# Kernel optimization log

Hardware: AMD Instinct MI355X
Metric: run time of the kernel (lower is better)

## Reference

```python
import jax, jax.numpy as jnp
import numpy as np

LAMBDA_SOFTMAX = 9.0
LAMBDA_LSE = 6.0
EPS = 1e-8
LEAKY_SLOPE = 0.1


def setup_inputs() -> dict:
    key = jax.random.key(0)
    k1, k2, k3, k4 = jax.random.split(key, 4)
    B, R, L, D = 256, 36, 40, 1024  # n_image=n_caption=B, n_regions, max_words, embed
    return {
        'pool_img': jax.random.normal(k1, (B, D), jnp.float32),
        'img_emb': jax.random.normal(k2, (B, R, D), jnp.float32),
        'pool_txt': jax.random.normal(k3, (B, D), jnp.float32),
        'cap_emb': jax.random.normal(k4, (B, L, D), jnp.float32),
    }


def _l2norm(x, axis):
    return x / (jnp.sqrt(jnp.sum(x * x, axis=axis, keepdims=True)) + EPS)


def _lse_reduce(m):
    # mul_(lambda_lse).exp_() ; sum over singleton dim ; log / lambda_lse
    return jnp.log(jnp.exp(m * LAMBDA_LSE)) / LAMBDA_LSE


def _text_score_one(cap_i, txt_poo_i, images):
    # cap_i: (L, d) query; images: (B, R, d) context. clipped_l2norm variant.
    attn = jnp.einsum('brd,ld->brl', images, cap_i)            # (B, R, L)
    attn = jax.nn.leaky_relu(attn, LEAKY_SLOPE)
    attn = _l2norm(attn, axis=2)                               # l2norm over queryL
    attn = jnp.swapaxes(attn, 1, 2)                            # (B, L, R)
    attn = jax.nn.softmax(attn * LAMBDA_SOFTMAX, axis=-1)      # softmax over regions
    wctx = jnp.einsum('blr,brd->bld', attn, images)            # (B, L, d)
    w12 = jnp.einsum('bld,d->bl', wctx, txt_poo_i)
    w1 = jnp.sqrt(jnp.sum(txt_poo_i * txt_poo_i))
    w2 = jnp.sqrt(jnp.sum(wctx * wctx, axis=2))
    sim = w12 / jnp.maximum(w1 * w2, EPS)                      # (B, L)
    return _lse_reduce(jnp.mean(sim, axis=1))                  # (B,)


def _image_score_one(cap_i, img_emb, img_poo):
    # query: img_emb (B, R, d); context: cap_i (L, d) broadcast over B.
    attn = jnp.einsum('ld,brd->blr', cap_i, img_emb)           # (B, L, R)
    attn = jax.nn.leaky_relu(attn, LEAKY_SLOPE)
    attn = _l2norm(attn, axis=2)                               # l2norm over regions
    attn = jnp.swapaxes(attn, 1, 2)                            # (B, R, L)
    attn = jax.nn.softmax(attn * LAMBDA_SOFTMAX, axis=-1)      # softmax over words
    wctx = jnp.einsum('brl,ld->brd', attn, cap_i)              # (B, R, d)
    w12 = jnp.einsum('brd,bd->br', wctx, img_poo)
    w1 = jnp.sqrt(jnp.sum(img_poo * img_poo, axis=1, keepdims=True))  # (B,1)
    w2 = jnp.sqrt(jnp.sum(wctx * wctx, axis=2))                # (B, R)
    sim = w12 / jnp.maximum(w1 * w2, EPS)
    return _lse_reduce(jnp.mean(sim, axis=1))                  # (B,)


def reference(pool_img, img_emb, pool_txt, cap_emb):
    # scores_t2i: loop over captions -> vmap; result (n_cap, n_image) -> transpose
    t2i = jax.vmap(_text_score_one, in_axes=(0, 0, None))(cap_emb, pool_txt, img_emb).T
    i2t = jax.vmap(_image_score_one, in_axes=(0, None, None))(cap_emb, img_emb, pool_img).T
    base = pool_img @ pool_txt.T
    return t2i + i2t + base
```

## Files before the change

### kernel.cpp

```cpp
#include <hip/hip_runtime.h>

typedef unsigned short u16;
typedef __attribute__((ext_vector_type(8))) short bf16x8;
typedef __attribute__((ext_vector_type(4))) float f32x4;
typedef __attribute__((ext_vector_type(4))) unsigned u32x4;

#define D_EMB 1024
#define NBAT  256
#define AS1 __attribute__((address_space(1)))
#define AS3 __attribute__((address_space(3)))

__device__ __forceinline__ u16 f2bf(float f){
    unsigned int u = __float_as_uint(f);
    unsigned int r = (u + 0x7fffu + ((u >> 16) & 1u)) >> 16;
    return (u16)r;
}
__device__ __forceinline__ float leaky(float x){ return x > 0.f ? x : 0.1f * x; }

__device__ __forceinline__ unsigned pack2(float a, float b){
    return (__float_as_uint(a) >> 16) | (__float_as_uint(b) & 0xffff0000u);
}

__global__ void pack_kernel(const float* __restrict__ pool_img, const float* __restrict__ img_emb,
                            const float* __restrict__ pool_txt, const float* __restrict__ cap_emb,
                            u16* __restrict__ imgw, u16* __restrict__ capw){
    int row = blockIdx.x;
    const float* src; u16* dst;
    if (row < NBAT * 37){
        int e = row / 37, rr = row - e * 37;
        src = (rr < 36) ? (img_emb + ((size_t)e * 36 + rr) * D_EMB) : (pool_img + (size_t)e * D_EMB);
        dst = imgw + (size_t)row * D_EMB;
    } else {
        int r2 = row - NBAT * 37;
        int e = r2 / 41, rr = r2 - e * 41;
        src = (rr < 40) ? (cap_emb + ((size_t)e * 40 + rr) * D_EMB) : (pool_txt + (size_t)e * D_EMB);
        dst = capw + (size_t)r2 * D_EMB;
    }
    int t = threadIdx.x;
    float4 v = ((const float4*)src)[t];
    unsigned long long pk = (unsigned long long)f2bf(v.x)
        | ((unsigned long long)f2bf(v.y) << 16)
        | ((unsigned long long)f2bf(v.z) << 32)
        | ((unsigned long long)f2bf(v.w) << 48);
    *(unsigned long long*)(dst + (size_t)t * 4) = pk;
}

__global__ void norm_kernel(const float* __restrict__ pool_img, const float* __restrict__ pool_txt,
                            float* __restrict__ w1i, float* __restrict__ w1t){
    __shared__ float red[256];
    int v = blockIdx.x;
    const float* src = (v < 256) ? (pool_img + (size_t)v * D_EMB)
                                 : (pool_txt + (size_t)(v - 256) * D_EMB);
    int t = threadIdx.x;
    float4 x = ((const float4*)src)[t];
    red[t] = x.x*x.x + x.y*x.y + x.z*x.z + x.w*x.w;
    __syncthreads();
    for (int off = 128; off > 0; off >>= 1){
        if (t < off) red[t] += red[t + off];
        __syncthreads();
    }
    if (t == 0){
        float n = sqrtf(red[0]);
        if (v < 256) w1i[v] = n; else w1t[v - 256] = n;
    }
}

__launch_bounds__(256, 2)
__global__ void gram_kernel(const u16* __restrict__ imgw, const u16* __restrict__ capw,
                            float* __restrict__ G, float* __restrict__ H){
    __shared__ __align__(16) char gsm[6144];
    int blk = blockIdx.x;
    int tid = threadIdx.x, lane = tid & 63;
    int wave = __builtin_amdgcn_readfirstlane(tid >> 6);
    int frow = lane & 15, q = lane >> 4;

    const u16* E; float* Gout; int R;
    if (blk < NBAT){ E = imgw + (size_t)blk * 37 * D_EMB; Gout = G + (size_t)blk * 1296; R = 36; }
    else { int b = blk - NBAT; E = capw + (size_t)b * 41 * D_EMB; Gout = H + (size_t)b * 1600; R = 40; }

    {
        uint4 z = {0u,0u,0u,0u};
        for (int off = tid * 16; off < 6144; off += 4096) *(uint4*)(gsm + off) = z;
    }

    const u16* gsrc[2]; int goff[2]; bool gval[2];
    #pragma unroll
    for (int j = 0; j < 2; ++j){
        int g = wave + j * 4;
        gval[j] = false; gsrc[j] = E; goff[j] = 0;
        if (g < 6){
            int kk = g / 3, t = g - kk * 3;
            int row = t * 16 + frow;
            gsrc[j] = E + (size_t)row * D_EMB + kk * 32 + q * 8;
            goff[j] = g * 1024;
            gval[j] = (row < R);
        }
    }

    int wm = wave >> 1, wn = wave & 1;
    int nTm = wm ? 1 : 2, nTn = wn ? 1 : 2;
    f32x4 acc[2][2];
    #pragma unroll
    for (int a = 0; a < 2; ++a)
        #pragma unroll
        for (int b = 0; b < 2; ++b) acc[a][b] = (f32x4){0.f,0.f,0.f,0.f};

    for (int c = 0; c < 16; ++c){
        __syncthreads();
        #pragma unroll
        for (int j = 0; j < 2; ++j){
            if (gval[j]){
                __builtin_amdgcn_global_load_lds(
                    (const AS1 void*)(const void*)(gsrc[j] + c * 64),
                    (AS3 void*)(void*)(gsm + goff[j] + lane * 16),
                    16, 0, 0);
            }
        }
        __syncthreads();
        #pragma unroll
        for (int kk = 0; kk < 2; ++kk){
            bf16x8 fA[2], fB[2];
            #pragma unroll
            for (int mi = 0; mi < 2; ++mi)
                if (mi < nTm) fA[mi] = *(const bf16x8*)(gsm + ((kk * 3 + (wm + mi * 2)) * 64 + lane) * 16);
            #pragma unroll
            for (int ni = 0; ni < 2; ++ni)
                if (ni < nTn) fB[ni] = *(const bf16x8*)(gsm + ((kk * 3 + (wn + ni * 2)) * 64 + lane) * 16);
            #pragma unroll
            for (int mi = 0; mi < 2; ++mi)
                if (mi < nTm)
                    #pragma unroll
                    for (int ni = 0; ni < 2; ++ni)
                        if (ni < nTn)
                            acc[mi][ni] = __builtin_amdgcn_mfma_f32_16x16x32_bf16(
                                fA[mi], fB[ni], acc[mi][ni], 0, 0, 0);
        }
    }

    #pragma unroll
    for (int mi = 0; mi < 2; ++mi){
        if (mi < nTm){
            int tm = wm + mi * 2;
            #pragma unroll
            for (int ni = 0; ni < 2; ++ni){
                if (ni < nTn){
                    int tn = wn + ni * 2;
                    int col = tn * 16 + frow;
                    if (col < R){
                        #pragma unroll
                        for (int g = 0; g < 4; ++g){
                            int row = tm * 16 + q * 4 + g;
                            if (row < R) Gout[row * R + col] = acc[mi][ni][g];
                        }
                    }
                }
            }
        }
    }
}

template<int R>
__device__ __forceinline__ void chol_wave(const float* __restrict__ src,
                                          u16* __restrict__ dst, int lane){
    int r = lane;
    bool act = (r < R);
    const float* row = src + (size_t)(act ? r : 0) * R;
    float a[R];
    #pragma unroll
    for (int k = 0; k < R; ++k) a[k] = act ? row[k] : 0.f;
    #pragma unroll
    for (int j = 0; j < R; ++j){
        float ajj = __shfl(a[j], j);
        float inv = (ajj > 1e-12f) ? rsqrtf(ajj) : 0.f;
        float lrj = a[j] * inv;
        if (r < j || !act) lrj = 0.f;
        dst[j * 64 + lane] = f2bf(lrj);
        #pragma unroll
        for (int k = j + 1; k < R; ++k){
            float lkj = __shfl(lrj, k);
            a[k] = fmaf(-lrj, lkj, a[k]);
        }
    }
    #pragma unroll
    for (int j = R; j < 48; ++j) dst[j * 64 + lane] = 0;
}

__global__ void chol_kernel(const float* __restrict__ G, const float* __restrict__ H,
                            u16* __restrict__ Lbi, u16* __restrict__ Lbc){
    int lane = threadIdx.x & 63;
    int wave = threadIdx.x >> 6;
    int id = blockIdx.x * 4 + wave;
    if (id < NBAT) chol_wave<36>(G + (size_t)id * 1296, Lbi + (size_t)id * 3072, lane);
    else           chol_wave<40>(H + (size_t)(id - NBAT) * 1600, Lbc + (size_t)(id - NBAT) * 3072, lane);
}

__launch_bounds__(256, 5)
__global__ void fused_kernel(const u16* __restrict__ imgw, const u16* __restrict__ capw,
                             const u16* __restrict__ Lbi, const u16* __restrict__ Lbc,
                             const float* __restrict__ w1i, const float* __restrict__ w1t,
                             float* __restrict__ out){
    __shared__ __align__(16) char smem[26624];
    float* Call = (float*)smem;
    float* rnb  = (float*)(smem + 25160);
    float* cnb  = (float*)(smem + 25736);

    int tid  = threadIdx.x;
    int lane = tid & 63;
    int wave = __builtin_amdgcn_readfirstlane(tid >> 6);
    int frow = lane & 15, q = lane >> 4;

    int lin = blockIdx.x;
    int xcd = lin & 7;
    int s   = lin >> 3;
    int b_t = (xcd << 4) | (s & 15);
    int i_t = s >> 4;
    int b0 = b_t * 2, i0 = i_t * 2;
    const u16* Ag = imgw + (size_t)b0 * 37 * D_EMB;
    const u16* Bg = capw + (size_t)i0 * 41 * D_EMB;

    {
        uint4 z = {0u,0u,0u,0u};
        for (int off = tid * 16; off < 22528; off += 4096) *(uint4*)(smem + off) = z;
    }

    const u16* gsrc[3]; int goff[3]; bool gval[3];
    #pragma unroll
    for (int j = 0; j < 3; ++j){
        int g = wave + j * 4;
        gval[j] = false; gsrc[j] = Ag; goff[j] = 0;
        if (g < 11){
            if (g < 5){
                int row = g * 16 + frow;
                gsrc[j] = Ag + (size_t)row * D_EMB + q * 8;
                goff[j] = g * 1024;
                gval[j] = (row < 74);
            } else {
                int gb = g - 5;
                int row = gb * 16 + frow;
                gsrc[j] = Bg + (size_t)row * D_EMB + q * 8;
                goff[j] = 5120 + gb * 1024;
                gval[j] = (row < 82);
            }
        }
    }

    int wm = wave >> 1, wn = wave & 1;
    int nTm = wm ? 2 : 3;
    f32x4 acc[3][3];
    #pragma unroll
    for (int aa = 0; aa < 3; ++aa)
        #pragma unroll
        for (int bb = 0; bb < 3; ++bb) acc[aa][bb] = (f32x4){0.f, 0.f, 0.f, 0.f};

    __syncthreads();

    #pragma unroll
    for (int j = 0; j < 3; ++j){
        if (gval[j]){
            __builtin_amdgcn_global_load_lds(
                (const AS1 void*)(const void*)(gsrc[j]),
                (AS3 void*)(void*)(smem + goff[j] + lane * 16),
                16, 0, 0);
        }
    }
    __syncthreads();

    for (int c = 0; c < 32; ++c){
        if (c < 31){
            int nb = ((c + 1) & 1) * 11264;
            #pragma unroll
            for (int j = 0; j < 3; ++j){
                if (gval[j]){
                    __builtin_amdgcn_global_load_lds(
                        (const AS1 void*)(const void*)(gsrc[j] + (c + 1) * 32),
                        (AS3 void*)(void*)(smem + nb + goff[j] + lane * 16),
                        16, 0, 0);
                }
            }
        }
        int cb = (c & 1) * 11264;
        bf16x8 bfr[3];
        #pragma unroll
        for (int ni = 0; ni < 3; ++ni){
            int tn = wn + ni * 2;
            bfr[ni] = *(const bf16x8*)(smem + cb + 5120 + tn * 1024 + lane * 16);
        }
        #pragma unroll
        for (int mi = 0; mi < 3; ++mi){
            if (mi < nTm){
                int tm = wm + mi * 2;
                bf16x8 af = *(const bf16x8*)(smem + cb + tm * 1024 + lane * 16);
                #pragma unroll
                for (int ni = 0; ni < 3; ++ni){
                    acc[mi][ni] = __builtin_amdgcn_mfma_f32_16x16x32_bf16(
                        af, bfr[ni], acc[mi][ni], 0, 0, 0);
                }
            }
        }
        __syncthreads();
    }

    #pragma unroll
    for (int mi = 0; mi < 3; ++mi){
        if (mi < nTm){
            int tm = wm + mi * 2;
            #pragma unroll
            for (int ni = 0; ni < 3; ++ni){
                int tn = wn + ni * 2;
                int col = tn * 16 + frow;
                int rbase = tm * 16 + q * 4;
                if (col < 82){
                    #pragma unroll
                    for (int g = 0; g < 4; ++g){
                        int rowc = rbase + g;
                        if (rowc < 74) Call[rowc * 85 + col] = acc[mi][ni][g];
                    }
                }
            }
        }
    }
    __syncthreads();

    int pb = wave >> 1, pi = wave & 1;
    int bg = b0 + pb, ig = i0 + pi;
    const float* Sv = Call + (pb * 37) * 85 + pi * 41;
    const u16* Lb_t2i = Lbi + (size_t)bg * 3072;
    const u16* Lb_i2t = Lbc + (size_t)ig * 3072;

    {
        int r0 = (lane < 36) ? lane : 35;
        float s2 = 0.f;
        #pragma unroll
        for (int l = 0; l < 40; ++l){ float x = leaky(Sv[r0 * 85 + l]); s2 = fmaf(x, x, s2); }
        if (lane < 36) rnb[wave * 36 + lane] = 1.f / (sqrtf(s2) + 1e-8f);
    }
    {
        int l0 = (lane < 40) ? lane : 39;
        float s2 = 0.f;
        #pragma unroll
        for (int r = 0; r < 36; ++r){ float x = leaky(Sv[r * 85 + l0]); s2 = fmaf(x, x, s2); }
        if (lane < 40) cnb[wave * 40 + lane] = 1.f / (sqrtf(s2) + 1e-8f);
    }
    float base = Sv[36 * 85 + 40];

    float tsum;
    {
        f32x4 pacc[3][3];
        #pragma unroll
        for (int aa = 0; aa < 3; ++aa)
            #pragma unroll
            for (int bb = 0; bb < 3; ++bb) pacc[aa][bb] = (f32x4){0.f,0.f,0.f,0.f};
        #pragma unroll
        for (int kk = 0; kk < 2; ++kk){
            float rn[8];
            #pragma unroll
            for (int j = 0; j < 8; ++j){
                int k = kk * 32 + q * 8 + j;
                int kc = (k < 36) ? k : 35;
                rn[j] = (k < 36) ? rnb[wave * 36 + kc] : 0.f;
            }
            u32x4 pw;
            #pragma unroll
            for (int jj = 0; jj < 4; ++jj){
                int k0 = kk * 32 + q * 8 + jj * 2, k1 = k0 + 1;
                int c0 = (k0 < 36) ? k0 : 35, c1 = (k1 < 36) ? k1 : 35;
                float p0 = (k0 < 36) ? Sv[c0 * 85 + 40] : 0.f;
                float p1 = (k1 < 36) ? Sv[c1 * 85 + 40] : 0.f;
                pw[jj] = pack2(p0, p1);
            }
            bf16x8 afr[3];
            #pragma unroll
            for (int mt = 0; mt < 3; ++mt){
                int m = mt * 16 + frow;
                u32x4 aw;
                #pragma unroll
                for (int jj = 0; jj < 4; ++jj){
                    int k0 = kk * 32 + q * 8 + jj * 2, k1 = k0 + 1;
                    int c0 = (k0 < 36) ? k0 : 35, c1 = (k1 < 36) ? k1 : 35;
                    float e0 = __expf(9.f * leaky(Sv[c0 * 85 + m]) * rn[jj * 2]);
                    float e1 = __expf(9.f * leaky(Sv[c1 * 85 + m]) * rn[jj * 2 + 1]);
                    e0 = (k0 < 36) ? e0 : 0.f;
                    e1 = (k1 < 36) ? e1 : 0.f;
                    aw[jj] = pack2(e0, e1);
                }
                afr[mt] = __builtin_bit_cast(bf16x8, aw);
            }
            #pragma unroll
            for (int nt = 0; nt < 3; ++nt){
                bf16x8 bfr = *(const bf16x8*)(Lb_t2i + (nt * 16 + frow) * 64 + kk * 32 + q * 8);
                if (nt == 2 && frow == 4) bfr = __builtin_bit_cast(bf16x8, pw);
                #pragma unroll
                for (int mt = 0; mt < 3; ++mt)
                    pacc[mt][nt] = __builtin_amdgcn_mfma_f32_16x16x32_bf16(
                        afr[mt], bfr, pacc[mt][nt], 0, 0, 0);
            }
        }
        float w1 = w1t[ig];
        tsum = 0.f;
        #pragma unroll
        for (int mt = 0; mt < 3; ++mt){
            #pragma unroll
            for (int g = 0; g < 4; ++g){
                float sv = pacc[mt][0][g] * pacc[mt][0][g]
                         + pacc[mt][1][g] * pacc[mt][1][g];
                float t2 = pacc[mt][2][g] * pacc[mt][2][g];
                sv += (frow < 4) ? t2 : 0.f;
                sv += __shfl_xor(sv, 1); sv += __shfl_xor(sv, 2);
                sv += __shfl_xor(sv, 4); sv += __shfl_xor(sv, 8);
                float nm = __shfl(pacc[mt][2][g], (lane & 48) + 4);
                int m = mt * 16 + 4 * q + g;
                float sim = nm / fmaxf(w1 * sqrtf(sv), 1e-8f);
                tsum += (m < 40) ? sim : 0.f;
            }
        }
        tsum += __shfl_xor(tsum, 16);
        tsum += __shfl_xor(tsum, 32);
    }

    float isum;
    {
        f32x4 pacc[3][3];
        #pragma unroll
        for (int aa = 0; aa < 3; ++aa)
            #pragma unroll
            for (int bb = 0; bb < 3; ++bb) pacc[aa][bb] = (f32x4){0.f,0.f,0.f,0.f};
        #pragma unroll
        for (int kk = 0; kk < 2; ++kk){
            float cn[8];
            #pragma unroll
            for (int j = 0; j < 8; ++j){
                int k = kk * 32 + q * 8 + j;
                int kc = (k < 40) ? k : 39;
                cn[j] = (k < 40) ? cnb[wave * 40 + kc] : 0.f;
            }
            u32x4 qw;
            #pragma unroll
            for (int jj = 0; jj < 4; ++jj){
                int k0 = kk * 32 + q * 8 + jj * 2, k1 = k0 + 1;
                int c0 = (k0 < 40) ? k0 : 39, c1 = (k1 < 40) ? k1 : 39;
                float q0 = (k0 < 40) ? Sv[36 * 85 + c0] : 0.f;
                float q1 = (k1 < 40) ? Sv[36 * 85 + c1] : 0.f;
                qw[jj] = pack2(q0, q1);
            }
            bf16x8 afr[3];
            #pragma unroll
            for (int mt = 0; mt < 3; ++mt){
                int m = mt * 16 + frow;
                int mr = (m < 36) ? m : 35;
                u32x4 aw;
                #pragma unroll
                for (int jj = 0; jj < 4; ++jj){
                    int k0 = kk * 32 + q * 8 + jj * 2, k1 = k0 + 1;
                    int c0 = (k0 < 40) ? k0 : 39, c1 = (k1 < 40) ? k1 : 39;
                    float e0 = __expf(9.f * leaky(Sv[mr * 85 + c0]) * cn[jj * 2]);
                    float e1 = __expf(9.f * leaky(Sv[mr * 85 + c1]) * cn[jj * 2 + 1]);
                    e0 = (k0 < 40) ? e0 : 0.f;
                    e1 = (k1 < 40) ? e1 : 0.f;
                    aw[jj] = pack2(e0, e1);
                }
                afr[mt] = __builtin_bit_cast(bf16x8, aw);
            }
            #pragma unroll
            for (int nt = 0; nt < 3; ++nt){
                bf16x8 bfr = *(const bf16x8*)(Lb_i2t + (nt * 16 + frow) * 64 + kk * 32 + q * 8);
                if (nt == 2 && frow == 8) bfr = __builtin_bit_cast(bf16x8, qw);
                #pragma unroll
                for (int mt = 0; mt < 3; ++mt)
                    pacc[mt][nt] = __builtin_amdgcn_mfma_f32_16x16x32_bf16(
                        afr[mt], bfr, pacc[mt][nt], 0, 0, 0);
            }
        }
        float w1 = w1i[bg];
        isum = 0.f;
        #pragma unroll
        for (int mt = 0; mt < 3; ++mt){
            #pragma unroll
            for (int g = 0; g < 4; ++g){
                float sv = pacc[mt][0][g] * pacc[mt][0][g]
                         + pacc[mt][1][g] * pacc[mt][1][g];
                float t2 = pacc[mt][2][g] * pacc[mt][2][g];
                sv += (frow < 8) ? t2 : 0.f;
                sv += __shfl_xor(sv, 1); sv += __shfl_xor(sv, 2);
                sv += __shfl_xor(sv, 4); sv += __shfl_xor(sv, 8);
                float nm = __shfl(pacc[mt][2][g], (lane & 48) + 8);
                int m = mt * 16 + 4 * q + g;
                float sim = nm / fmaxf(w1 * sqrtf(sv), 1e-8f);
                isum += (m < 36) ? sim : 0.f;
            }
        }
        isum += __shfl_xor(isum, 16);
        isum += __shfl_xor(isum, 32);
    }

    if (lane == 0)
        out[bg * 256 + ig] = tsum * (1.f / 40.f) + isum * (1.f / 36.f) + base;
}

extern "C" void kernel_launch(void* const* d_in, const int* in_sizes, int n_in,
                              void* d_out, int out_size, void* d_ws, size_t ws_size,
                              hipStream_t stream){
    const float* pool_img = (const float*)d_in[0];
    const float* img_emb  = (const float*)d_in[1];
    const float* pool_txt = (const float*)d_in[2];
    const float* cap_emb  = (const float*)d_in[3];
    float* out = (float*)d_out;

    char* ws = (char*)d_ws;
    size_t o = 0;
    u16* imgw = (u16*)(ws + o);  o += (size_t)256 * 37 * 1024 * 2;
    u16* capw = (u16*)(ws + o);  o += (size_t)256 * 41 * 1024 * 2;
    float* G  = (float*)(ws + o); o += (size_t)256 * 36 * 36 * 4;
    float* H  = (float*)(ws + o); o += (size_t)256 * 40 * 40 * 4;
    float* w1i = (float*)(ws + o); o += 1024;
    float* w1t = (float*)(ws + o); o += 1024;
    u16* Lbi = (u16*)(ws + o); o += (size_t)256 * 48 * 64 * 2;
    u16* Lbc = (u16*)(ws + o); o += (size_t)256 * 48 * 64 * 2;

    pack_kernel<<<19968, 256, 0, stream>>>(pool_img, img_emb, pool_txt, cap_emb, imgw, capw);
    norm_kernel<<<512, 256, 0, stream>>>(pool_img, pool_txt, w1i, w1t);
    gram_kernel<<<512, 256, 0, stream>>>(imgw, capw, G, H);
    chol_kernel<<<128, 256, 0, stream>>>(G, H, Lbi, Lbc);
    fused_kernel<<<16384, 256, 0, stream>>>(imgw, capw, Lbi, Lbc, w1i, w1t, out);
}
```

Measured before the change: 809.5 us.

## Fuse pool norms into pack, widen fused GEMM K-step, fold softmax scale

Computes the pooled-vector norms inside pack_kernel, which removes the separate norm kernel launch. Rewrites the fused kernel's main loop to load 64-wide K chunks, two MFMA k-slices per stage, in 16 iterations with single buffering instead of 32 double-buffered steps, so there are fewer barriers but less load/compute overlap. It also folds the softmax factor of 9 into the reciprocal norms, removing a multiply per exp. A clamp on the column index guards the out-of-range row reads.

```diff
diff --git a/kernel.cpp b/kernel.cpp
--- a/kernel.cpp
+++ b/kernel.cpp
@@ -23,18 +23,25 @@
 
 __global__ void pack_kernel(const float* __restrict__ pool_img, const float* __restrict__ img_emb,
                             const float* __restrict__ pool_txt, const float* __restrict__ cap_emb,
-                            u16* __restrict__ imgw, u16* __restrict__ capw){
+                            u16* __restrict__ imgw, u16* __restrict__ capw,
+                            float* __restrict__ w1i, float* __restrict__ w1t){
+    __shared__ float red[256];
     int row = blockIdx.x;
     const float* src; u16* dst;
+    bool is_pool; float* wout;
     if (row < NBAT * 37){
         int e = row / 37, rr = row - e * 37;
+        is_pool = (rr == 36);
         src = (rr < 36) ? (img_emb + ((size_t)e * 36 + rr) * D_EMB) : (pool_img + (size_t)e * D_EMB);
         dst = imgw + (size_t)row * D_EMB;
+        wout = w1i + e;
     } else {
         int r2 = row - NBAT * 37;
         int e = r2 / 41, rr = r2 - e * 41;
+        is_pool = (rr == 40);
         src = (rr < 40) ? (cap_emb + ((size_t)e * 40 + rr) * D_EMB) : (pool_txt + (size_t)e * D_EMB);
         dst = capw + (size_t)r2 * D_EMB;
+        wout = w1t + e;
     }
     int t = threadIdx.x;
     float4 v = ((const float4*)src)[t];
@@ -43,25 +50,14 @@
         | ((unsigned long long)f2bf(v.z) << 32)
         | ((unsigned long long)f2bf(v.w) << 48);
     *(unsigned long long*)(dst + (size_t)t * 4) = pk;
-}
-
-__global__ void norm_kernel(const float* __restrict__ pool_img, const float* __restrict__ pool_txt,
-                            float* __restrict__ w1i, float* __restrict__ w1t){
-    __shared__ float red[256];
-    int v = blockIdx.x;
-    const float* src = (v < 256) ? (pool_img + (size_t)v * D_EMB)
-                                 : (pool_txt + (size_t)(v - 256) * D_EMB);
-    int t = threadIdx.x;
-    float4 x = ((const float4*)src)[t];
-    red[t] = x.x*x.x + x.y*x.y + x.z*x.z + x.w*x.w;
-    __syncthreads();
-    for (int off = 128; off > 0; off >>= 1){
-        if (t < off) red[t] += red[t + off];
+    if (is_pool){
+        red[t] = v.x*v.x + v.y*v.y + v.z*v.z + v.w*v.w;
         __syncthreads();
-    }
-    if (t == 0){
-        float n = sqrtf(red[0]);
-        if (v < 256) w1i[v] = n; else w1t[v - 256] = n;
+        for (int off = 128; off > 0; off >>= 1){
+            if (t < off) red[t] += red[t + off];
+            __syncthreads();
+        }
+        if (t == 0) *wout = sqrtf(red[0]);
     }
 }
 
@@ -223,22 +219,24 @@
         for (int off = tid * 16; off < 22528; off += 4096) *(uint4*)(smem + off) = z;
     }
 
-    const u16* gsrc[3]; int goff[3]; bool gval[3];
-    #pragma unroll
-    for (int j = 0; j < 3; ++j){
+    const u16* gsrc[6]; int goff[6]; bool gval[6];
+    #pragma unroll
+    for (int j = 0; j < 6; ++j){
         int g = wave + j * 4;
         gval[j] = false; gsrc[j] = Ag; goff[j] = 0;
-        if (g < 11){
-            if (g < 5){
-                int row = g * 16 + frow;
-                gsrc[j] = Ag + (size_t)row * D_EMB + q * 8;
+        if (g < 22){
+            if (g < 10){
+                int tm = g % 5, kk = g / 5;
+                int row = tm * 16 + frow;
+                gsrc[j] = Ag + (size_t)row * D_EMB + kk * 32 + q * 8;
                 goff[j] = g * 1024;
                 gval[j] = (row < 74);
             } else {
-                int gb = g - 5;
-                int row = gb * 16 + frow;
-                gsrc[j] = Bg + (size_t)row * D_EMB + q * 8;
-                goff[j] = 5120 + gb * 1024;
+                int gb = g - 10;
+                int tn = gb % 6, kk = gb / 6;
+                int row = tn * 16 + frow;
+                gsrc[j] = Bg + (size_t)row * D_EMB + kk * 32 + q * 8;
+                goff[j] = 10240 + gb * 1024;
                 gval[j] = (row < 82);
             }
         }
@@ -252,53 +250,41 @@
         #pragma unroll
         for (int bb = 0; bb < 3; ++bb) acc[aa][bb] = (f32x4){0.f, 0.f, 0.f, 0.f};
 
+    for (int c = 0; c < 16; ++c){
+        __syncthreads();
+        #pragma unroll
+        for (int j = 0; j < 6; ++j){
+            if (gval[j]){
+                __builtin_amdgcn_global_load_lds(
+                    (const AS1 void*)(const void*)(gsrc[j] + c * 64),
+                    (AS3 void*)(void*)(smem + goff[j] + lane * 16),
+                    16, 0, 0);
+            }
+        }
+        __syncthreads();
+        #pragma unroll
+        for (int kk = 0; kk < 2; ++kk){
+            bf16x8 bfr[3];
+            #pragma unroll
+            for (int ni = 0; ni < 3; ++ni){
+                int tn = wn + ni * 2;
+                bfr[ni] = *(const bf16x8*)(smem + 10240 + ((kk * 6 + tn) * 64 + lane) * 16);
+            }
+            #pragma unroll
+            for (int mi = 0; mi < 3; ++mi){
+                if (mi < nTm){
+                    int tm = wm + mi * 2;
+                    bf16x8 af = *(const bf16x8*)(smem + ((kk * 5 + tm) * 64 + lane) * 16);
+                    #pragma unroll
+                    for (int ni = 0; ni < 3; ++ni){
+                        acc[mi][ni] = __builtin_amdgcn_mfma_f32_16x16x32_bf16(
+                            af, bfr[ni], acc[mi][ni], 0, 0, 0);
+                    }
+                }
+            }
+        }
+    }
     __syncthreads();
-
-    #pragma unroll
-    for (int j = 0; j < 3; ++j){
-        if (gval[j]){
-            __builtin_amdgcn_global_load_lds(
-                (const AS1 void*)(const void*)(gsrc[j]),
-                (AS3 void*)(void*)(smem + goff[j] + lane * 16),
-                16, 0, 0);
-        }
-    }
-    __syncthreads();
-
-    for (int c = 0; c < 32; ++c){
-        if (c < 31){
-            int nb = ((c + 1) & 1) * 11264;
-            #pragma unroll
-            for (int j = 0; j < 3; ++j){
-                if (gval[j]){
-                    __builtin_amdgcn_global_load_lds(
-                        (const AS1 void*)(const void*)(gsrc[j] + (c + 1) * 32),
-                        (AS3 void*)(void*)(smem + nb + goff[j] + lane * 16),
-                        16, 0, 0);
-                }
-            }
-        }
-        int cb = (c & 1) * 11264;
-        bf16x8 bfr[3];
-        #pragma unroll
-        for (int ni = 0; ni < 3; ++ni){
-            int tn = wn + ni * 2;
-            bfr[ni] = *(const bf16x8*)(smem + cb + 5120 + tn * 1024 + lane * 16);
-        }
-        #pragma unroll
-        for (int mi = 0; mi < 3; ++mi){
-            if (mi < nTm){
-                int tm = wm + mi * 2;
-                bf16x8 af = *(const bf16x8*)(smem + cb + tm * 1024 + lane * 16);
-                #pragma unroll
-                for (int ni = 0; ni < 3; ++ni){
-                    acc[mi][ni] = __builtin_amdgcn_mfma_f32_16x16x32_bf16(
-                        af, bfr[ni], acc[mi][ni], 0, 0, 0);
-                }
-            }
-        }
-        __syncthreads();
-    }
 
     #pragma unroll
     for (int mi = 0; mi < 3; ++mi){
@@ -332,14 +318,14 @@
         float s2 = 0.f;
         #pragma unroll
         for (int l = 0; l < 40; ++l){ float x = leaky(Sv[r0 * 85 + l]); s2 = fmaf(x, x, s2); }
-        if (lane < 36) rnb[wave * 36 + lane] = 1.f / (sqrtf(s2) + 1e-8f);
+        if (lane < 36) rnb[wave * 36 + lane] = 9.f / (sqrtf(s2) + 1e-8f);
     }
     {
         int l0 = (lane < 40) ? lane : 39;
         float s2 = 0.f;
         #pragma unroll
         for (int r = 0; r < 36; ++r){ float x = leaky(Sv[r * 85 + l0]); s2 = fmaf(x, x, s2); }
-        if (lane < 40) cnb[wave * 40 + lane] = 1.f / (sqrtf(s2) + 1e-8f);
+        if (lane < 40) cnb[wave * 40 + lane] = 9.f / (sqrtf(s2) + 1e-8f);
     }
     float base = Sv[36 * 85 + 40];
 
@@ -372,13 +358,14 @@
             #pragma unroll
             for (int mt = 0; mt < 3; ++mt){
                 int m = mt * 16 + frow;
+                int mc = (m < 40) ? m : 39;
                 u32x4 aw;
                 #pragma unroll
                 for (int jj = 0; jj < 4; ++jj){
                     int k0 = kk * 32 + q * 8 + jj * 2, k1 = k0 + 1;
                     int c0 = (k0 < 36) ? k0 : 35, c1 = (k1 < 36) ? k1 : 35;
-                    float e0 = __expf(9.f * leaky(Sv[c0 * 85 + m]) * rn[jj * 2]);
-                    float e1 = __expf(9.f * leaky(Sv[c1 * 85 + m]) * rn[jj * 2 + 1]);
+                    float e0 = __expf(leaky(Sv[c0 * 85 + mc] * rn[jj * 2]));
+                    float e1 = __expf(leaky(Sv[c1 * 85 + mc] * rn[jj * 2 + 1]));
                     e0 = (k0 < 36) ? e0 : 0.f;
                     e1 = (k1 < 36) ? e1 : 0.f;
                     aw[jj] = pack2(e0, e1);
@@ -452,8 +439,8 @@
                 for (int jj = 0; jj < 4; ++jj){
                     int k0 = kk * 32 + q * 8 + jj * 2, k1 = k0 + 1;
                     int c0 = (k0 < 40) ? k0 : 39, c1 = (k1 < 40) ? k1 : 39;
-                    float e0 = __expf(9.f * leaky(Sv[mr * 85 + c0]) * cn[jj * 2]);
-                    float e1 = __expf(9.f * leaky(Sv[mr * 85 + c1]) * cn[jj * 2 + 1]);
+                    float e0 = __expf(leaky(Sv[mr * 85 + c0] * cn[jj * 2]));
+                    float e1 = __expf(leaky(Sv[mr * 85 + c1] * cn[jj * 2 + 1]));
                     e0 = (k0 < 40) ? e0 : 0.f;
                     e1 = (k1 < 40) ? e1 : 0.f;
                     aw[jj] = pack2(e0, e1);
@@ -516,8 +503,8 @@
     u16* Lbi = (u16*)(ws + o); o += (size_t)256 * 48 * 64 * 2;
     u16* Lbc = (u16*)(ws + o); o += (size_t)256 * 48 * 64 * 2;
 
-    pack_kernel<<<19968, 256, 0, stream>>>(pool_img, img_emb, pool_txt, cap_emb, imgw, capw);
-    norm_kernel<<<512, 256, 0, stream>>>(pool_img, pool_txt, w1i, w1t);
+    pack_kernel<<<19968, 256, 0, stream>>>(pool_img, img_emb, pool_txt, cap_emb,
+                                           imgw, capw, w1i, w1t);
     gram_kernel<<<512, 256, 0, stream>>>(imgw, capw, G, H);
     chol_kernel<<<128, 256, 0, stream>>>(G, H, Lbi, Lbc);
     fused_kernel<<<16384, 256, 0, stream>>>(imgw, capw, Lbi, Lbc, w1i, w1t, out);
```

Measured after the change: 806.8 us. About the same (-0.3%).
